# Kernel optimization log

Hardware: AMD Instinct MI355X
Metric: run time of the kernel (lower is better)

## Reference

```python
import jax, jax.numpy as jnp
import numpy as np
from jax import lax

B, C, H, W = 8, 256, 128, 128


def _scan_along(x, decay, axis):
    """Linear decay recurrence s_t = decay*s_{t-1} + (1-decay)*x_t along `axis`.

    x: [B, C, H, W]; decay: [C] (constant per channel).
    """
    xm = jnp.moveaxis(x, axis, 0)          # [L, B, C, rest]
    d = decay.reshape(1, -1, 1)            # broadcast over [B, C, rest]
    one_minus_d = 1.0 - d

    def step(state, cur):
        state = d * state + one_minus_d * cur
        return state, state

    init = jnp.zeros_like(xm[0])
    _, ys = lax.scan(step, init, xm)
    return jnp.moveaxis(ys, 0, axis)


def setup_inputs() -> dict:
    key = jax.random.key(0)
    k1, k2, k3, k4 = jax.random.split(key, 4)
    x = jax.random.normal(k1, (B, C, H, W), dtype=jnp.float32)
    decay_logits = 0.5 * jax.random.normal(k2, (4, C), dtype=jnp.float32)
    mix_logits = 0.5 * jax.random.normal(k3, (4, C), dtype=jnp.float32)
    input_scale = 0.5 * jax.random.normal(k4, (4, C), dtype=jnp.float32)
    return {"x": x, "decay_logits": decay_logits,
            "mix_logits": mix_logits, "input_scale": input_scale}


def reference(x, decay_logits, mix_logits, input_scale):
    decay = jnp.clip(jax.nn.sigmoid(decay_logits), 0.05, 0.995)   # [4, C]
    mix = jax.nn.softmax(mix_logits, axis=0)                       # [4, C]
    scale = 1.0 + jnp.tanh(input_scale)                            # [4, C]

    def sc(d):  # per-channel [C] -> broadcastable [1, C, 1, 1]
        return d.reshape(1, -1, 1, 1)

    # left -> right: scan along width (axis 3)
    lr = _scan_along(x * sc(scale[0]), decay[0], axis=3)
    # right -> left: flip width, scan, flip back
    rl = jnp.flip(_scan_along(jnp.flip(x, axis=3) * sc(scale[1]), decay[1], axis=3), axis=3)
    # top -> bottom: scan along height (axis 2)
    tb = _scan_along(x * sc(scale[2]), decay[2], axis=2)
    # bottom -> top: flip height, scan, flip back
    bt = jnp.flip(_scan_along(jnp.flip(x, axis=2) * sc(scale[3]), decay[3], axis=2), axis=2)

    return sc(mix[0]) * lr + sc(mix[1]) * rl + sc(mix[2]) * tb + sc(mix[3]) * bt
```

## Files before the change

### kernel.cpp

```cpp
#include <hip/hip_runtime.h>

#define CH 256
#define HH 128
#define WW 128
#define HW (HH * WW)
#define SEGH 16
#define NSEG 8

__global__ __launch_bounds__(1024, 4) void dscan_kernel(
    const float* __restrict__ x,
    const float* __restrict__ decay_logits,
    const float* __restrict__ mix_logits,
    const float* __restrict__ input_scale,
    float* __restrict__ out)
{
    extern __shared__ float smem[];
    float* __restrict__ xs  = smem;
    float* __restrict__ scr = smem + HW;

    const int img  = blockIdx.x;
    const int c    = img & (CH - 1);
    const int tid  = threadIdx.x;
    const int lane = tid & 63;
    const int wv   = tid >> 6;

    const float dl0 = decay_logits[0 * CH + c];
    const float dl1 = decay_logits[1 * CH + c];
    const float dl2 = decay_logits[2 * CH + c];
    const float dl3 = decay_logits[3 * CH + c];
    const float ml0 = mix_logits[0 * CH + c];
    const float ml1 = mix_logits[1 * CH + c];
    const float ml2 = mix_logits[2 * CH + c];
    const float ml3 = mix_logits[3 * CH + c];
    const float il0 = input_scale[0 * CH + c];
    const float il1 = input_scale[1 * CH + c];
    const float il2 = input_scale[2 * CH + c];
    const float il3 = input_scale[3 * CH + c];

    const float d0 = fminf(fmaxf(1.0f / (1.0f + expf(-dl0)), 0.05f), 0.995f);
    const float d1 = fminf(fmaxf(1.0f / (1.0f + expf(-dl1)), 0.05f), 0.995f);
    const float d2 = fminf(fmaxf(1.0f / (1.0f + expf(-dl2)), 0.05f), 0.995f);
    const float d3 = fminf(fmaxf(1.0f / (1.0f + expf(-dl3)), 0.05f), 0.995f);

    const float mmax = fmaxf(fmaxf(ml0, ml1), fmaxf(ml2, ml3));
    const float e0 = expf(ml0 - mmax);
    const float e1 = expf(ml1 - mmax);
    const float e2 = expf(ml2 - mmax);
    const float e3 = expf(ml3 - mmax);
    const float einv = 1.0f / (e0 + e1 + e2 + e3);
    const float m0 = e0 * einv, m1 = e1 * einv, m2 = e2 * einv, m3 = e3 * einv;

    const float sc0 = 1.0f + tanhf(il0);
    const float sc1 = 1.0f + tanhf(il1);
    const float sc2 = 1.0f + tanhf(il2);
    const float sc3 = 1.0f + tanhf(il3);

    const float c0 = (1.0f - d0) * sc0;
    const float c1 = (1.0f - d1) * sc1;
    const float c2 = (1.0f - d2) * sc2;
    const float c3 = (1.0f - d3) * sc3;

    const float d0p4 = (d0 * d0) * (d0 * d0);
    const float d1p4 = (d1 * d1) * (d1 * d1);
    float q0[5], q1[5];
    q0[0] = d0p4; q1[0] = d1p4;
#pragma unroll
    for (int k = 1; k < 5; ++k) { q0[k] = q0[k-1] * q0[k-1]; q1[k] = q1[k-1] * q1[k-1]; }

    float t2 = d2 * d2; t2 = t2 * t2; t2 = t2 * t2; const float d2p16 = t2 * t2;
    float t3 = d3 * d3; t3 = t3 * t3; t3 = t3 * t3; const float d3p16 = t3 * t3;

    const float* __restrict__ xg = x + (size_t)img * HW;
    float* __restrict__ og = out + (size_t)img * HW;

    {
        const int sl   = lane & 31;
        const int half = lane >> 5;
        const int rbase = (wv << 1) + half;

        float4 v[4];
#pragma unroll
        for (int it = 0; it < 4; ++it)
            v[it] = *(const float4*)(xg + ((it << 5) + rbase) * WW + (sl << 2));

#pragma unroll
        for (int it = 0; it < 4; ++it) {
            const int r = (it << 5) + rbase;
            const float4 xv4 = v[it];

            float bL = c0 * xv4.x;
            bL = fmaf(d0, bL, c0 * xv4.y);
            bL = fmaf(d0, bL, c0 * xv4.z);
            bL = fmaf(d0, bL, c0 * xv4.w);
            float bR = c1 * xv4.w;
            bR = fmaf(d1, bR, c1 * xv4.z);
            bR = fmaf(d1, bR, c1 * xv4.y);
            bR = fmaf(d1, bR, c1 * xv4.x);

#pragma unroll
            for (int k = 0; k < 5; ++k) {
                const int off = 1 << k;
                const float bU = __shfl_up(bL, (unsigned)off, 32);
                bL = fmaf(q0[k], (sl >= off) ? bU : 0.0f, bL);
                const float bD = __shfl_down(bR, (unsigned)off, 32);
                bR = fmaf(q1[k], (sl < 32 - off) ? bD : 0.0f, bR);
            }
            float EL = __shfl_up(bL, 1u, 32);
            if (sl == 0) EL = 0.0f;
            float ER = __shfl_down(bR, 1u, 32);
            if (sl == 31) ER = 0.0f;

            const float l0 = fmaf(d0, EL, c0 * xv4.x);
            const float l1 = fmaf(d0, l0, c0 * xv4.y);
            const float l2 = fmaf(d0, l1, c0 * xv4.z);
            const float l3 = fmaf(d0, l2, c0 * xv4.w);
            const float r3 = fmaf(d1, ER, c1 * xv4.w);
            const float r2 = fmaf(d1, r3, c1 * xv4.z);
            const float r1 = fmaf(d1, r2, c1 * xv4.y);
            const float r0 = fmaf(d1, r1, c1 * xv4.x);

            float4 o4;
            o4.x = fmaf(m0, l0, m1 * r0);
            o4.y = fmaf(m0, l1, m1 * r1);
            o4.z = fmaf(m0, l2, m1 * r2);
            o4.w = fmaf(m0, l3, m1 * r3);
            *(float4*)(xs + r * WW + (sl << 2)) = o4;
        }
    }

    const int col = tid & (WW - 1);
    const int seg = tid >> 7;
    const float* __restrict__ xcol = xg + seg * SEGH * WW + col;
    {
        float b2 = 0.0f, b3 = 0.0f, pw = c3;
#pragma unroll
        for (int i = 0; i < SEGH; ++i) {
            const float xv = xcol[i * WW];
            b2 = fmaf(d2, b2, c2 * xv);
            b3 = fmaf(pw, xv, b3);
            pw *= d3;
        }
        scr[tid]        = b2;
        scr[1024 + tid] = b3;
    }

    __syncthreads();

    float Sin = 0.0f;
    for (int j = 0; j < seg; ++j)
        Sin = fmaf(d2p16, Sin, scr[j * WW + col]);
    float Tin = 0.0f;
    for (int j = NSEG - 1; j > seg; --j)
        Tin = fmaf(d3p16, Tin, scr[1024 + j * WW + col]);

    {
        float xv[SEGH], tb[SEGH];
        float s = Sin;
#pragma unroll
        for (int i = 0; i < SEGH; ++i) {
            const float v = xcol[i * WW];
            xv[i] = v;
            s = fmaf(d2, s, c2 * v);
            tb[i] = s;
        }
        float t = Tin;
        float* __restrict__ ocol = og + seg * SEGH * WW + col;
        const float* __restrict__ pcol = xs + seg * SEGH * WW + col;
#pragma unroll
        for (int i = SEGH - 1; i >= 0; --i) {
            t = fmaf(d3, t, c3 * xv[i]);
            const float hres = pcol[i * WW];
            ocol[i * WW] = fmaf(m2, tb[i], fmaf(m3, t, hres));
        }
    }
}

extern "C" void kernel_launch(void* const* d_in, const int* in_sizes, int n_in,
                              void* d_out, int out_size, void* d_ws, size_t ws_size,
                              hipStream_t stream) {
    const float* x  = (const float*)d_in[0];
    const float* dl = (const float*)d_in[1];
    const float* ml = (const float*)d_in[2];
    const float* is = (const float*)d_in[3];
    float* out = (float*)d_out;

    const size_t lds_bytes = (size_t)(HW + 2048) * sizeof(float);

    static bool attr_set = false;
    if (!attr_set) {
        (void)hipFuncSetAttribute((const void*)dscan_kernel,
                                  hipFuncAttributeMaxDynamicSharedMemorySize,
                                  (int)lds_bytes);
        attr_set = true;
    }

    dim3 grid(2048), block(1024);
    hipLaunchKernelGGL(dscan_kernel, grid, block, lds_bytes, stream, x, dl, ml, is, out);
}
```

Measured before the change: 245.4 us.

## Stage input tile in LDS once and write output with row-wise float4 stores

The image tile is now loaded from global memory once with float4 loads and staged in LDS. The vertical scans read their columns from LDS instead of issuing two strided global reads. The vertical result is written back into LDS, and the horizontal pass adds it and stores the output as coalesced float4 rows instead of column-strided scalar stores. This costs an extra __syncthreads and more LDS traffic, and register pressure rises from keeping both v[4] and tmp[16] live.

```diff
diff --git a/kernel.cpp b/kernel.cpp
--- a/kernel.cpp
+++ b/kernel.cpp
@@ -73,105 +73,107 @@
     const float* __restrict__ xg = x + (size_t)img * HW;
     float* __restrict__ og = out + (size_t)img * HW;
 
+    const int sl    = lane & 31;
+    const int half  = lane >> 5;
+    const int rbase = (wv << 1) + half;
+    const int cb    = sl << 2;
+
+    float4 v[4];
+#pragma unroll
+    for (int it = 0; it < 4; ++it) {
+        const int r = (it << 5) + rbase;
+        v[it] = *(const float4*)(xg + r * WW + cb);
+        *(float4*)(xs + r * WW + cb) = v[it];
+    }
+    __syncthreads();
+
+    const int col  = tid & (WW - 1);
+    const int seg  = tid >> 7;
+    const int base = seg * SEGH * WW + col;
+
+    float tmp[SEGH];
+#pragma unroll
+    for (int i = 0; i < SEGH; ++i) tmp[i] = xs[base + i * WW];
+
     {
-        const int sl   = lane & 31;
-        const int half = lane >> 5;
-        const int rbase = (wv << 1) + half;
-
-        float4 v[4];
-#pragma unroll
-        for (int it = 0; it < 4; ++it)
-            v[it] = *(const float4*)(xg + ((it << 5) + rbase) * WW + (sl << 2));
-
-#pragma unroll
-        for (int it = 0; it < 4; ++it) {
-            const int r = (it << 5) + rbase;
-            const float4 xv4 = v[it];
-
-            float bL = c0 * xv4.x;
-            bL = fmaf(d0, bL, c0 * xv4.y);
-            bL = fmaf(d0, bL, c0 * xv4.z);
-            bL = fmaf(d0, bL, c0 * xv4.w);
-            float bR = c1 * xv4.w;
-            bR = fmaf(d1, bR, c1 * xv4.z);
-            bR = fmaf(d1, bR, c1 * xv4.y);
-            bR = fmaf(d1, bR, c1 * xv4.x);
-
-#pragma unroll
-            for (int k = 0; k < 5; ++k) {
-                const int off = 1 << k;
-                const float bU = __shfl_up(bL, (unsigned)off, 32);
-                bL = fmaf(q0[k], (sl >= off) ? bU : 0.0f, bL);
-                const float bD = __shfl_down(bR, (unsigned)off, 32);
-                bR = fmaf(q1[k], (sl < 32 - off) ? bD : 0.0f, bR);
-            }
-            float EL = __shfl_up(bL, 1u, 32);
-            if (sl == 0) EL = 0.0f;
-            float ER = __shfl_down(bR, 1u, 32);
-            if (sl == 31) ER = 0.0f;
-
-            const float l0 = fmaf(d0, EL, c0 * xv4.x);
-            const float l1 = fmaf(d0, l0, c0 * xv4.y);
-            const float l2 = fmaf(d0, l1, c0 * xv4.z);
-            const float l3 = fmaf(d0, l2, c0 * xv4.w);
-            const float r3 = fmaf(d1, ER, c1 * xv4.w);
-            const float r2 = fmaf(d1, r3, c1 * xv4.z);
-            const float r1 = fmaf(d1, r2, c1 * xv4.y);
-            const float r0 = fmaf(d1, r1, c1 * xv4.x);
-
-            float4 o4;
-            o4.x = fmaf(m0, l0, m1 * r0);
-            o4.y = fmaf(m0, l1, m1 * r1);
-            o4.z = fmaf(m0, l2, m1 * r2);
-            o4.w = fmaf(m0, l3, m1 * r3);
-            *(float4*)(xs + r * WW + (sl << 2)) = o4;
-        }
-    }
-
-    const int col = tid & (WW - 1);
-    const int seg = tid >> 7;
-    const float* __restrict__ xcol = xg + seg * SEGH * WW + col;
-    {
-        float b2 = 0.0f, b3 = 0.0f, pw = c3;
-#pragma unroll
-        for (int i = 0; i < SEGH; ++i) {
-            const float xv = xcol[i * WW];
-            b2 = fmaf(d2, b2, c2 * xv);
-            b3 = fmaf(pw, xv, b3);
-            pw *= d3;
-        }
+        float b2 = 0.0f;
+#pragma unroll
+        for (int i = 0; i < SEGH; ++i) b2 = fmaf(d2, b2, c2 * tmp[i]);
+        float b3 = 0.0f;
+#pragma unroll
+        for (int i = SEGH - 1; i >= 0; --i) b3 = fmaf(d3, b3, c3 * tmp[i]);
         scr[tid]        = b2;
         scr[1024 + tid] = b3;
     }
-
     __syncthreads();
 
-    float Sin = 0.0f;
-    for (int j = 0; j < seg; ++j)
-        Sin = fmaf(d2p16, Sin, scr[j * WW + col]);
-    float Tin = 0.0f;
-    for (int j = NSEG - 1; j > seg; --j)
-        Tin = fmaf(d3p16, Tin, scr[1024 + j * WW + col]);
-
     {
-        float xv[SEGH], tb[SEGH];
+        float Sin = 0.0f;
+        for (int j = 0; j < seg; ++j)
+            Sin = fmaf(d2p16, Sin, scr[j * WW + col]);
+        float Tin = 0.0f;
+        for (int j = NSEG - 1; j > seg; --j)
+            Tin = fmaf(d3p16, Tin, scr[1024 + j * WW + col]);
+
+        float vc[SEGH];
+        float t = Tin;
+#pragma unroll
+        for (int i = SEGH - 1; i >= 0; --i) {
+            t = fmaf(d3, t, c3 * tmp[i]);
+            vc[i] = m3 * t;
+        }
         float s = Sin;
 #pragma unroll
         for (int i = 0; i < SEGH; ++i) {
-            const float v = xcol[i * WW];
-            xv[i] = v;
-            s = fmaf(d2, s, c2 * v);
-            tb[i] = s;
+            s = fmaf(d2, s, c2 * tmp[i]);
+            xs[base + i * WW] = fmaf(m2, s, vc[i]);
         }
-        float t = Tin;
-        float* __restrict__ ocol = og + seg * SEGH * WW + col;
-        const float* __restrict__ pcol = xs + seg * SEGH * WW + col;
-#pragma unroll
-        for (int i = SEGH - 1; i >= 0; --i) {
-            t = fmaf(d3, t, c3 * xv[i]);
-            const float hres = pcol[i * WW];
-            ocol[i * WW] = fmaf(m2, tb[i], fmaf(m3, t, hres));
+    }
+    __syncthreads();
+
+#pragma unroll
+    for (int it = 0; it < 4; ++it) {
+        const int r = (it << 5) + rbase;
+        const float4 xv4 = v[it];
+        const float4 vc4 = *(const float4*)(xs + r * WW + cb);
+
+        float bL = c0 * xv4.x;
+        bL = fmaf(d0, bL, c0 * xv4.y);
+        bL = fmaf(d0, bL, c0 * xv4.z);
+        bL = fmaf(d0, bL, c0 * xv4.w);
+        float bR = c1 * xv4.w;
+        bR = fmaf(d1, bR, c1 * xv4.z);
+        bR = fmaf(d1, bR, c1 * xv4.y);
+        bR = fmaf(d1, bR, c1 * xv4.x);
+
+#pragma unroll
+        for (int k = 0; k < 5; ++k) {
+            const int off = 1 << k;
+            const float bU = __shfl_up(bL, (unsigned)off, 32);
+            bL = fmaf(q0[k], (sl >= off) ? bU : 0.0f, bL);
+            const float bD = __shfl_down(bR, (unsigned)off, 32);
+            bR = fmaf(q1[k], (sl < 32 - off) ? bD : 0.0f, bR);
         }
+        float EL = __shfl_up(bL, 1u, 32);
+        if (sl == 0) EL = 0.0f;
+        float ER = __shfl_down(bR, 1u, 32);
+        if (sl == 31) ER = 0.0f;
+
+        const float l0 = fmaf(d0, EL, c0 * xv4.x);
+        const float l1 = fmaf(d0, l0, c0 * xv4.y);
+        const float l2 = fmaf(d0, l1, c0 * xv4.z);
+        const float l3 = fmaf(d0, l2, c0 * xv4.w);
+        const float r3 = fmaf(d1, ER, c1 * xv4.w);
+        const float r2 = fmaf(d1, r3, c1 * xv4.z);
+        const float r1 = fmaf(d1, r2, c1 * xv4.y);
+        const float r0 = fmaf(d1, r1, c1 * xv4.x);
+
+        float4 o4;
+        o4.x = vc4.x + fmaf(m0, l0, m1 * r0);
+        o4.y = vc4.y + fmaf(m0, l1, m1 * r1);
+        o4.z = vc4.z + fmaf(m0, l2, m1 * r2);
+        o4.w = vc4.w + fmaf(m0, l3, m1 * r3);
+        *(float4*)(og + r * WW + cb) = o4;
     }
 }
 
```

Result: no change. 249.1 us (+1.5%).
